# Kernel tuning notes

Hardware: AMD Instinct MI355X
Metric: run time of the kernel (lower is better)

Reference implementation:

```python
import jax, jax.numpy as jnp
import numpy as np

V = 100000          # vocab size
D = 256             # hidden dim
B, N = 32, 128      # batch, max_len
K = 100             # noise_ratio
NORM_TERM = 11.512925  # log(V), norm_term='auto'
BACKOFF_PROB = 1e-10


def setup_inputs() -> dict:
    key = jax.random.key(0)
    ks = jax.random.split(key, 6)
    target = jax.random.randint(ks[0], (B, N), 0, V)
    noise_samples = jax.random.randint(ks[1], (B, N, K), 0, V)
    hidden = jax.random.normal(ks[2], (B, N, D), dtype=jnp.float32) * 0.1
    weight = jax.random.normal(ks[3], (V, D), dtype=jnp.float32) * 0.05
    bias = jax.random.normal(ks[4], (V,), dtype=jnp.float32) * 0.01
    u = jax.random.uniform(ks[5], (V,), dtype=jnp.float32) + BACKOFF_PROB
    noise_probs = u / jnp.sum(u)  # normalized noise distribution
    return {"target": target, "noise_samples": noise_samples, "hidden": hidden,
            "weight": weight, "bias": bias, "noise_probs": noise_probs}


def reference(target, noise_samples, hidden, weight, bias, noise_probs):
    # score_noise = log P_noise(noise_samples)   (B,N,K) -- irregular gather on (V,)
    score_noise = jnp.log(noise_probs)[noise_samples]
    # get_score (IndexLinear): gathered output-embedding dot products
    w_t = weight[target]                                   # (B,N,D)
    score_model = jnp.einsum('bnd,bnd->bn', hidden, w_t) + bias[target] - NORM_TERM
    w_n = weight[noise_samples]                            # (B,N,K,D) big gather
    score_noise_in_model = (jnp.einsum('bnd,bnkd->bnk', hidden, w_n)
                            + bias[noise_samples] - NORM_TERM)
    # NCE binary classification loss (score_target_in_noise passed as zeros)
    log_k = jnp.log(jnp.float32(K))
    logit_true = score_model - log_k                        # (B,N) label=1
    logit_noise = score_noise_in_model - score_noise - log_k  # (B,N,K) label=0
    # BCE-with-logits: -log sigmoid(x) = softplus(-x); -log(1-sigmoid(x)) = softplus(x)
    loss = jax.nn.softplus(-logit_true) + jnp.sum(jax.nn.softplus(logit_noise), axis=-1)
    # reduction='elementwise_mean'
    return jnp.mean(loss)
```

## Files before the change

### kernel.cpp

```cpp
#include <hip/hip_runtime.h>
#include <math.h>

#define V 100000
#define D 256
#define B 32
#define N 128
#define K 100
#define NPOS (B * N)
#define NORM_TERM 11.512925f
#define LOG_K 4.605170186f

__device__ __forceinline__ float softplus(float x) {
    return fmaxf(x, 0.f) + log1pf(expf(-fabsf(x)));
}

__global__ __launch_bounds__(128) void nce_kernel(
    const int* __restrict__ target,
    const int* __restrict__ noise,
    const float* __restrict__ hidden,
    const float* __restrict__ weight,
    const float* __restrict__ bias,
    const float* __restrict__ noise_probs,
    float* __restrict__ out)
{
    const int pos = blockIdx.x;
    const int tid = threadIdx.x;
    const float* __restrict__ hrow = hidden + (size_t)pos * D;

    float loss = 0.f;
    if (tid <= K) {
        const int idx = (tid < K) ? noise[(size_t)pos * K + tid] : target[pos];
        const float* __restrict__ wrow = weight + (size_t)idx * D;

        float ax = 0.f, ay = 0.f, az = 0.f, aw = 0.f;
        #pragma unroll 4
        for (int d = 0; d < D; d += 4) {
            const float4 w4 = *reinterpret_cast<const float4*>(wrow + d);
            ax = fmaf(w4.x, hrow[d + 0], ax);
            ay = fmaf(w4.y, hrow[d + 1], ay);
            az = fmaf(w4.z, hrow[d + 2], az);
            aw = fmaf(w4.w, hrow[d + 3], aw);
        }
        const float dot = (ax + ay) + (az + aw);
        const float score = dot + bias[idx] - NORM_TERM;

        if (tid < K) {
            loss = softplus(score - logf(noise_probs[idx]) - LOG_K);
        } else {
            loss = softplus(LOG_K - score);
        }
    }

    #pragma unroll
    for (int off = 32; off >= 1; off >>= 1)
        loss += __shfl_xor(loss, off, 64);

    __shared__ float wsum[2];
    if ((tid & 63) == 0) wsum[tid >> 6] = loss;
    __syncthreads();
    if (tid == 0)
        atomicAdd(out, (wsum[0] + wsum[1]) * (1.0f / (float)NPOS));
}

extern "C" void kernel_launch(void* const* d_in, const int* in_sizes, int n_in,
                              void* d_out, int out_size, void* d_ws, size_t ws_size,
                              hipStream_t stream) {
    const int*   target      = (const int*)d_in[0];
    const int*   noise       = (const int*)d_in[1];
    const float* hidden      = (const float*)d_in[2];
    const float* weight      = (const float*)d_in[3];
    const float* bias        = (const float*)d_in[4];
    const float* noise_probs = (const float*)d_in[5];
    float* out = (float*)d_out;

    hipMemsetAsync(out, 0, sizeof(float), stream);

    nce_kernel<<<NPOS, 128, 0, stream>>>(target, noise, hidden, weight,
                                         bias, noise_probs, out);
}
```

Before: 237.8 us.

## Cooperative 16-lane row gather with coalesced loads and fast math softplus

```diff
diff --git a/kernel.cpp b/kernel.cpp
--- a/kernel.cpp
+++ b/kernel.cpp
@@ -7,11 +7,12 @@
 #define N 128
 #define K 100
 #define NPOS (B * N)
+#define NGROUPS 26
 #define NORM_TERM 11.512925f
 #define LOG_K 4.605170186f
 
 __device__ __forceinline__ float softplus(float x) {
-    return fmaxf(x, 0.f) + log1pf(expf(-fabsf(x)));
+    return fmaxf(x, 0.f) + __logf(1.f + __expf(-fabsf(x)));
 }
 
 __global__ __launch_bounds__(128) void nce_kernel(
@@ -23,40 +24,57 @@
     const float* __restrict__ noise_probs,
     float* __restrict__ out)
 {
-    const int pos = blockIdx.x;
-    const int tid = threadIdx.x;
+    const int pos  = blockIdx.x;
+    const int tid  = threadIdx.x;
+    const int wave = tid >> 6;
+    const int lane = tid & 63;
+    const int q    = lane >> 4;
+    const int ql   = lane & 15;
+
     const float* __restrict__ hrow = hidden + (size_t)pos * D;
+    float4 hreg[4];
+    #pragma unroll
+    for (int i = 0; i < 4; ++i)
+        hreg[i] = *reinterpret_cast<const float4*>(hrow + ql * 4 + i * 64);
 
     float loss = 0.f;
-    if (tid <= K) {
-        const int idx = (tid < K) ? noise[(size_t)pos * K + tid] : target[pos];
-        const float* __restrict__ wrow = weight + (size_t)idx * D;
+    for (int g = wave; g < NGROUPS; g += 2) {
+        const int r = g * 4 + q;
+        const bool is_noise  = (r < K);
+        const bool is_target = (r == K);
 
-        float ax = 0.f, ay = 0.f, az = 0.f, aw = 0.f;
-        #pragma unroll 4
-        for (int d = 0; d < D; d += 4) {
-            const float4 w4 = *reinterpret_cast<const float4*>(wrow + d);
-            ax = fmaf(w4.x, hrow[d + 0], ax);
-            ay = fmaf(w4.y, hrow[d + 1], ay);
-            az = fmaf(w4.z, hrow[d + 2], az);
-            aw = fmaf(w4.w, hrow[d + 3], aw);
+        int idx = 0;
+        if (is_noise)       idx = noise[(size_t)pos * K + r];
+        else if (is_target) idx = target[pos];
+
+        const float* __restrict__ wrow = weight + (size_t)idx * D + ql * 4;
+        float acc = 0.f;
+        #pragma unroll
+        for (int i = 0; i < 4; ++i) {
+            const float4 w4 = *reinterpret_cast<const float4*>(wrow + i * 64);
+            acc = fmaf(w4.x, hreg[i].x, acc);
+            acc = fmaf(w4.y, hreg[i].y, acc);
+            acc = fmaf(w4.z, hreg[i].z, acc);
+            acc = fmaf(w4.w, hreg[i].w, acc);
         }
-        const float dot = (ax + ay) + (az + aw);
-        const float score = dot + bias[idx] - NORM_TERM;
+        #pragma unroll
+        for (int off = 1; off < 16; off <<= 1)
+            acc += __shfl_xor(acc, off, 64);
 
-        if (tid < K) {
-            loss = softplus(score - logf(noise_probs[idx]) - LOG_K);
-        } else {
-            loss = softplus(LOG_K - score);
-        }
+        const float score = acc + bias[idx] - NORM_TERM;
+        float contrib = 0.f;
+        if (is_noise)
+            contrib = softplus(score - __logf(noise_probs[idx]) - LOG_K);
+        else if (is_target)
+            contrib = softplus(LOG_K - score);
+        if (ql == 0) loss += contrib;
     }
 
-    #pragma unroll
-    for (int off = 32; off >= 1; off >>= 1)
-        loss += __shfl_xor(loss, off, 64);
+    loss += __shfl_xor(loss, 16, 64);
+    loss += __shfl_xor(loss, 32, 64);
 
     __shared__ float wsum[2];
-    if ((tid & 63) == 0) wsum[tid >> 6] = loss;
+    if (lane == 0) wsum[wave] = loss;
     __syncthreads();
     if (tid == 0)
         atomicAdd(out, (wsum[0] + wsum[1]) * (1.0f / (float)NPOS));
```

Measured after the change: 240.9 us. Within noise of the previous version (+1.3%).
